# Kernel optimization log

Hardware: AMD Instinct MI355X
Metric: run time of the kernel (lower is better)

Reference implementation:

```python
import jax, jax.numpy as jnp
import numpy as np

H = 512
E = 300
V = 32000
B, L, T = 32, 64, 32

def setup_inputs() -> dict:
    key = jax.random.key(0)
    ks = jax.random.split(key, 24)
    n = jax.random.normal
    inp = {
        "enc_h": n(ks[0], (B, L, 2 * H), jnp.float32),
        "prev_s": n(ks[1], (B, H), jnp.float32),
        "target_word": jax.random.randint(ks[2], (B, T), 0, V),
        # frozen embedding table
        "embed": n(ks[3], (V, E), jnp.float32) * 0.1,
        # attention: W_a (HxH), U_a (2H->H), linear (H->1)
        "W_a": n(ks[4], (H, H), jnp.float32) * 0.001,
        "b_a": jnp.zeros((H,), jnp.float32),
        "U_a": n(ks[5], (2 * H, H), jnp.float32) * 0.001,
        "b_Ua": jnp.zeros((H,), jnp.float32),
        "v_w": n(ks[6], (H,), jnp.float32) * 0.01,
        "v_b": jnp.zeros((1,), jnp.float32),
        # decoder cell, gates stacked as [z | r | s] along output dim
        "W_emb": n(ks[7], (E, 3 * H), jnp.float32) * 0.01,
        "b_emb": jnp.zeros((3 * H,), jnp.float32),
        "W_hid_zr": n(ks[8], (H, 2 * H), jnp.float32) * 0.01,
        "b_hid_zr": jnp.zeros((2 * H,), jnp.float32),
        "W_hid_s": n(ks[9], (H, H), jnp.float32) * 0.01,
        "b_hid_s": jnp.zeros((H,), jnp.float32),
        "W_ctx": n(ks[10], (2 * H, 3 * H), jnp.float32) * 0.01,
        "b_ctx": jnp.zeros((3 * H,), jnp.float32),
        # hid2word
        "W_out": n(ks[11], (H, V), jnp.float32) * 0.02,
        "b_out": jnp.zeros((V,), jnp.float32),
    }
    return inp

def _decode(enc_h, prev_s, target_word, embed, W_a, b_a, U_a, b_Ua, v_w, v_b,
            W_emb, b_emb, W_hid_zr, b_hid_zr, W_hid_s, b_hid_s, W_ctx, b_ctx,
            W_out, b_out):
    # enc_h: B x L x 2H. Precompute U_a(enc_h) once (loop-invariant).
    Uh = jnp.einsum('bld,dh->blh', enc_h, U_a) + b_Ua  # B x L x H
    target_emb = embed[target_word]                    # B x T x E (frozen)

    def step(s, emb_t):
        # Bahdanau attention
        out_s = s @ W_a + b_a                                   # B x H
        scores = jnp.tanh(out_s[:, None, :] + Uh) @ v_w + v_b   # B x L
        attn = jax.nn.softmax(scores, axis=1)                   # B x L
        ctx = jnp.einsum('bld,bl->bd', enc_h, attn)             # B x 2H
        # GRU-like cell, gates stacked [z | r | s]
        ge = emb_t @ W_emb + b_emb          # B x 3H
        gh = s @ W_hid_zr + b_hid_zr        # B x 2H (z, r)
        gc = ctx @ W_ctx + b_ctx            # B x 3H
        z = jax.nn.sigmoid(ge[:, :H] + gh[:, :H] + gc[:, :H])
        r = jax.nn.sigmoid(ge[:, H:2 * H] + gh[:, H:] + gc[:, H:2 * H])
        s_tilde = jnp.tanh(ge[:, 2 * H:] + (r * s) @ W_hid_s + b_hid_s + gc[:, 2 * H:])
        s_new = (1.0 - z) * s + z * s_tilde
        return s_new, s_new

    _, s_seq = jax.lax.scan(step, prev_s, jnp.swapaxes(target_emb, 0, 1))
    s_seq = jnp.swapaxes(s_seq, 0, 1)                # B x T x H
    return jnp.einsum('bth,hv->btv', s_seq, W_out) + b_out  # B x T x V

def reference(enc_h, prev_s, target_word, embed, W_a, b_a, U_a, b_Ua, v_w, v_b,
              W_emb, b_emb, W_hid_zr, b_hid_zr, W_hid_s, b_hid_s, W_ctx, b_ctx,
              W_out, b_out):
    return _decode(enc_h, prev_s, target_word, embed, W_a, b_a, U_a, b_Ua, v_w, v_b,
                   W_emb, b_emb, W_hid_zr, b_hid_zr, W_hid_s, b_hid_s, W_ctx, b_ctx,
                   W_out, b_out)
```

## Files before the change

kernel.cpp:

```cpp
#include <hip/hip_runtime.h>
#include <cstdint>

#define HH   512
#define HD2  1024
#define HD3  1536
#define EE   300
#define VV   32000
#define BB   32
#define LLn  64
#define TT   32

typedef unsigned short u16;
typedef __attribute__((ext_vector_type(8))) short short8;
typedef __attribute__((ext_vector_type(4))) float f32x4;

__device__ __forceinline__ float fast_tanh(float x) {
    float e = __expf(2.f * x);
    return 1.f - 2.f / (e + 1.f);
}
__device__ __forceinline__ float fast_sigmoid(float x) {
    float e = __expf(-x);
    return 1.f / (1.f + e);
}
__device__ __forceinline__ u16 f2bf(float x) {
    union { float f; unsigned u; } v; v.f = x;
    unsigned r = v.u + 0x7FFFu + ((v.u >> 16) & 1u);
    return (u16)(r >> 16);
}

__global__ __launch_bounds__(256) void conv_hilo(
    const float* __restrict__ src, const int* __restrict__ gather,
    int rows_out, int cols_out, int rows_valid, int cols_valid,
    u16* __restrict__ hi, u16* __restrict__ lo)
{
    int idx = blockIdx.x * 256 + threadIdx.x;
    if (idx >= rows_out * cols_out) return;
    int r = idx / cols_out, c = idx - r * cols_out;
    float x = 0.f;
    if (r < rows_valid && c < cols_valid) {
        int sr = gather ? gather[r] : r;
        x = src[(size_t)sr * cols_valid + c];
    }
    union { float f; unsigned u; } v; v.f = x;
    unsigned uh = v.u & 0xFFFF0000u;
    float res = x - __uint_as_float(uh);
    union { float f; unsigned u; } w; w.f = res;
    hi[idx] = (u16)(v.u >> 16);
    lo[idx] = (u16)(w.u >> 16);
}

template<int KSTEPS>
__global__ __launch_bounds__(256) void pre_mfma(
    const u16* __restrict__ Ahi, const u16* __restrict__ Alo,
    const u16* __restrict__ Whi, const u16* __restrict__ Wlo,
    const float* __restrict__ bias, float* __restrict__ C, int N)
{
    __shared__ u16 ah[256 * 40], al[256 * 40];
    __shared__ u16 bh[64 * 40],  bl[64 * 40];
    const int nb = blockIdx.x, mb = blockIdx.y, tid = threadIdx.x;
    const int w = tid >> 6, ln = tid & 63;
    const int quad = ln >> 4, lm = ln & 15;
    const int n0 = nb * 64;
    const int K = KSTEPS * 32;

    f32x4 acc[4][4];
#pragma unroll
    for (int r = 0; r < 4; r++)
#pragma unroll
        for (int c = 0; c < 4; c++)
            acc[r][c] = (f32x4){0.f, 0.f, 0.f, 0.f};

    for (int kt = 0; kt < KSTEPS; kt++) {
        const int k0 = kt * 32;
        {
            const uint4* sh = (const uint4*)(Ahi + (size_t)(mb * 256 + tid) * K + k0);
            const uint4* sl = (const uint4*)(Alo + (size_t)(mb * 256 + tid) * K + k0);
            uint4 h0 = sh[0], h1 = sh[1], h2 = sh[2], h3 = sh[3];
            uint4 l0 = sl[0], l1 = sl[1], l2 = sl[2], l3 = sl[3];
            uint4* dh = (uint4*)(ah + tid * 40);
            dh[0] = h0; dh[1] = h1; dh[2] = h2; dh[3] = h3;
            uint4* dl = (uint4*)(al + tid * 40);
            dl[0] = l0; dl[1] = l1; dl[2] = l2; dl[3] = l3;
        }
        {
            const int kr = tid >> 3, c8 = (tid & 7) * 8;
            union { uint4 v; u16 u[8]; } uh, ul;
            uh.v = *(const uint4*)(Whi + (size_t)(k0 + kr) * N + n0 + c8);
            ul.v = *(const uint4*)(Wlo + (size_t)(k0 + kr) * N + n0 + c8);
#pragma unroll
            for (int j = 0; j < 8; j++) {
                bh[(c8 + j) * 40 + kr] = uh.u[j];
                bl[(c8 + j) * 40 + kr] = ul.u[j];
            }
        }
        __syncthreads();
        short8 afh[4], afl[4], bfh[4], bfl[4];
#pragma unroll
        for (int r = 0; r < 4; r++) {
            afh[r] = *(const short8*)(ah + ((w * 4 + r) * 16 + lm) * 40 + quad * 8);
            afl[r] = *(const short8*)(al + ((w * 4 + r) * 16 + lm) * 40 + quad * 8);
        }
#pragma unroll
        for (int c = 0; c < 4; c++) {
            bfh[c] = *(const short8*)(bh + (c * 16 + lm) * 40 + quad * 8);
            bfl[c] = *(const short8*)(bl + (c * 16 + lm) * 40 + quad * 8);
        }
#pragma unroll
        for (int r = 0; r < 4; r++)
#pragma unroll
            for (int c = 0; c < 4; c++) {
                acc[r][c] = __builtin_amdgcn_mfma_f32_16x16x32_bf16(
                    afh[r], bfh[c], acc[r][c], 0, 0, 0);
                acc[r][c] = __builtin_amdgcn_mfma_f32_16x16x32_bf16(
                    afh[r], bfl[c], acc[r][c], 0, 0, 0);
                acc[r][c] = __builtin_amdgcn_mfma_f32_16x16x32_bf16(
                    afl[r], bfh[c], acc[r][c], 0, 0, 0);
            }
        __syncthreads();
    }
#pragma unroll
    for (int r = 0; r < 4; r++) {
        int row = mb * 256 + (w * 4 + r) * 16 + quad * 4;
#pragma unroll
        for (int c = 0; c < 4; c++) {
            int col = n0 + c * 16 + lm;
            float bo = bias[col];
#pragma unroll
            for (int q2 = 0; q2 < 4; q2++)
                C[(size_t)(row + q2) * N + col] = acc[r][c][q2] + bo;
        }
    }
}

__global__ __launch_bounds__(256) void step_a(
    const float* __restrict__ s_buf, const float* __restrict__ W_a,
    const float* __restrict__ W_hzr, float* __restrict__ parts1)
{
    __shared__ float s_lds[64 * 8];
    const int jt = blockIdx.x, p = blockIdx.y, bq = blockIdx.z;
    const int tid = threadIdx.x;
    const int kk  = tid & 63, blq = tid >> 6;
    const int k0  = p * 64, b0 = bq * 8;

#pragma unroll
    for (int i = 0; i < 2; i++) {
        int bl = blq * 2 + i;
        s_lds[kk * 8 + bl] = s_buf[(b0 + bl) * HH + k0 + kk];
    }
    __syncthreads();

    const int j = jt * 256 + tid;
    const float* Wp; int ld;
    if (j < HH) { Wp = W_a + j;          ld = HH;  }
    else        { Wp = W_hzr + (j - HH); ld = HD2; }
    Wp += (size_t)k0 * ld;

    float acc[8];
#pragma unroll
    for (int r = 0; r < 8; r++) acc[r] = 0.f;
    for (int k = 0; k < 64; k++) {
        float w = Wp[(size_t)k * ld];
#pragma unroll
        for (int r = 0; r < 2; r++) {
            float4 s4 = *(const float4*)(s_lds + k * 8 + r * 4);
            acc[r * 4 + 0] = fmaf(s4.x, w, acc[r * 4 + 0]);
            acc[r * 4 + 1] = fmaf(s4.y, w, acc[r * 4 + 1]);
            acc[r * 4 + 2] = fmaf(s4.z, w, acc[r * 4 + 2]);
            acc[r * 4 + 3] = fmaf(s4.w, w, acc[r * 4 + 3]);
        }
    }
#pragma unroll
    for (int r = 0; r < 8; r++)
        parts1[((size_t)p * BB + b0 + r) * HD3 + j] = acc[r];
}

__global__ __launch_bounds__(256) void step_b(
    const float* __restrict__ parts1, const float* __restrict__ Uh,
    const float* __restrict__ Gc, const float* __restrict__ Ge,
    const float* __restrict__ W_hs,
    const float* __restrict__ b_a, const float* __restrict__ v_w,
    const float* __restrict__ v_b, const float* __restrict__ b_hzr,
    const float* __restrict__ b_hs,
    const float* __restrict__ s_prev, float* __restrict__ s_next,
    u16* __restrict__ sseq, int t)
{
    const int b = blockIdx.x, q = blockIdx.y, tid = threadIdx.x;
    __shared__ float outs[HH];
    __shared__ float red[256];
    __shared__ float attn_s[LLn];
    __shared__ float rs_s[HH];
    __shared__ float zb_s[128], pst_s[128];

    for (int h = tid; h < HH; h += 256) {
        float a = b_a[h];
#pragma unroll
        for (int p = 0; p < 8; p++)
            a += parts1[((size_t)p * BB + b) * HD3 + h];
        outs[h] = a;
    }
    __syncthreads();

    {
        const int l = tid & 63, jj = tid >> 6;
        const float* uh = Uh + ((size_t)b * LLn + l) * HH + jj * 128;
        const float* os = outs + jj * 128;
        const float* vw = v_w + jj * 128;
        float acc = 0.f;
#pragma unroll 8
        for (int i = 0; i < 128; i++)
            acc = fmaf(fast_tanh(os[i] + uh[i]), vw[i], acc);
        red[tid] = acc;
    }
    __syncthreads();

    if (tid < 64) {
        float v = red[tid] + red[64 + tid] + red[128 + tid] + red[192 + tid] + v_b[0];
        float m = v;
        for (int o = 32; o > 0; o >>= 1) m = fmaxf(m, __shfl_xor(m, o));
        float e = __expf(v - m);
        float s = e;
        for (int o = 32; o > 0; o >>= 1) s += __shfl_xor(s, o);
        attn_s[tid] = e / s;
    }
    __syncthreads();

    const float* ge = Ge + (size_t)(b * TT + t) * HD3;

    {
        float g1a = 0.f, g1b = 0.f;
        const float* gc = Gc + (size_t)b * LLn * HD3 + HH;
#pragma unroll 4
        for (int l = 0; l < LLn; l++) {
            float a = attn_s[l];
            g1a = fmaf(a, gc[(size_t)l * HD3 + tid],       g1a);
            g1b = fmaf(a, gc[(size_t)l * HD3 + tid + 256], g1b);
        }
        float gra = b_hzr[HH + tid]       + ge[HH + tid]       + g1a;
        float grb = b_hzr[HH + tid + 256] + ge[HH + tid + 256] + g1b;
#pragma unroll
        for (int p = 0; p < 8; p++) {
            const float* pp = parts1 + ((size_t)p * BB + b) * HD3;
            gra += pp[HD2 + tid];
            grb += pp[HD2 + tid + 256];
        }
        rs_s[tid]       = fast_sigmoid(gra) * s_prev[b * HH + tid];
        rs_s[tid + 256] = fast_sigmoid(grb) * s_prev[b * HH + tid + 256];
    }

    {
        const int hq = q * 128 + (tid & 127);
        if (tid < 128) {
            float g0 = 0.f;
            const float* gc = Gc + (size_t)b * LLn * HD3;
#pragma unroll 4
            for (int l = 0; l < LLn; l++)
                g0 = fmaf(attn_s[l], gc[(size_t)l * HD3 + hq], g0);
            float gz = b_hzr[hq] + ge[hq] + g0;
#pragma unroll
            for (int p = 0; p < 8; p++)
                gz += parts1[((size_t)p * BB + b) * HD3 + HH + hq];
            zb_s[tid] = fast_sigmoid(gz);
        } else {
            float g2 = 0.f;
            const float* gc = Gc + (size_t)b * LLn * HD3 + HD2;
#pragma unroll 4
            for (int l = 0; l < LLn; l++)
                g2 = fmaf(attn_s[l], gc[(size_t)l * HD3 + hq], g2);
            pst_s[tid - 128] = ge[HD2 + hq] + g2 + b_hs[hq];
        }
    }
    __syncthreads();

    {
        const int c = tid & 127, half = tid >> 7;
        const int h0 = q * 128 + c;
        const float* wp = W_hs + (size_t)(half * 256) * HH + h0;
        const float* rp = rs_s + half * 256;
        float a0 = 0.f, a1 = 0.f, a2 = 0.f, a3 = 0.f;
#pragma unroll 4
        for (int k = 0; k < 256; k += 4) {
            a0 = fmaf(rp[k + 0], wp[(size_t)(k + 0) * HH], a0);
            a1 = fmaf(rp[k + 1], wp[(size_t)(k + 1) * HH], a1);
            a2 = fmaf(rp[k + 2], wp[(size_t)(k + 2) * HH], a2);
            a3 = fmaf(rp[k + 3], wp[(size_t)(k + 3) * HH], a3);
        }
        red[tid] = (a0 + a1) + (a2 + a3);
    }
    __syncthreads();

    if (tid < 128) {
        const int h0 = q * 128 + tid;
        float tot = red[tid] + red[128 + tid];
        float st  = fast_tanh(pst_s[tid] + tot);
        float sv  = s_prev[b * HH + h0];
        float sn  = fmaf(zb_s[tid], st - sv, sv);
        s_next[b * HH + h0] = sn;
        sseq[((size_t)b * TT + t) * HH + h0] = f2bf(sn);
    }
}

__global__ __launch_bounds__(256) void final_gemm(
    const u16* __restrict__ Abf, const float* __restrict__ Wout,
    const float* __restrict__ b_out, float* __restrict__ out)
{
    __shared__ u16 a_lds[256 * 40];
    __shared__ u16 b_lds[64 * 40];
    const int nb = blockIdx.x, mb = blockIdx.y, tid = threadIdx.x;
    const int w = tid >> 6, ln = tid & 63;
    const int quad = ln >> 4, lm = ln & 15;
    const int n0 = nb * 64;

    f32x4 acc[4][4];
#pragma unroll
    for (int r = 0; r < 4; r++)
#pragma unroll
        for (int c = 0; c < 4; c++)
            acc[r][c] = (f32x4){0.f, 0.f, 0.f, 0.f};

    for (int kt = 0; kt < 16; kt++) {
        const int k0 = kt * 32;
        {
            const uint4* src = (const uint4*)(Abf + ((size_t)(mb * 256 + tid)) * HH + k0);
            uint4 v0 = src[0], v1 = src[1], v2 = src[2], v3 = src[3];
            uint4* dst = (uint4*)(a_lds + tid * 40);
            dst[0] = v0; dst[1] = v1; dst[2] = v2; dst[3] = v3;
        }
        {
            int kr = tid >> 3, c8 = (tid & 7) * 8;
            const float4* wp = (const float4*)(Wout + (size_t)(k0 + kr) * VV + n0 + c8);
            float4 f0 = wp[0], f1 = wp[1];
            u16 u[8] = { f2bf(f0.x), f2bf(f0.y), f2bf(f0.z), f2bf(f0.w),
                         f2bf(f1.x), f2bf(f1.y), f2bf(f1.z), f2bf(f1.w) };
#pragma unroll
            for (int j = 0; j < 8; j++)
                b_lds[(c8 + j) * 40 + kr] = u[j];
        }
        __syncthreads();
        short8 af[4], bfr[4];
#pragma unroll
        for (int r = 0; r < 4; r++)
            af[r] = *(const short8*)(a_lds + ((w * 4 + r) * 16 + lm) * 40 + quad * 8);
#pragma unroll
        for (int c = 0; c < 4; c++)
            bfr[c] = *(const short8*)(b_lds + (c * 16 + lm) * 40 + quad * 8);
#pragma unroll
        for (int r = 0; r < 4; r++)
#pragma unroll
            for (int c = 0; c < 4; c++)
                acc[r][c] = __builtin_amdgcn_mfma_f32_16x16x32_bf16(
                    af[r], bfr[c], acc[r][c], 0, 0, 0);
        __syncthreads();
    }
#pragma unroll
    for (int r = 0; r < 4; r++) {
        int row = mb * 256 + (w * 4 + r) * 16 + quad * 4;
#pragma unroll
        for (int c = 0; c < 4; c++) {
            int col = n0 + c * 16 + lm;
            float bo = b_out[col];
#pragma unroll
            for (int q = 0; q < 4; q++)
                out[(size_t)(row + q) * VV + col] = acc[r][c][q] + bo;
        }
    }
}

extern "C" void kernel_launch(void* const* d_in, const int* in_sizes, int n_in,
                              void* d_out, int out_size, void* d_ws, size_t ws_size,
                              hipStream_t stream)
{
    const float* enc_h  = (const float*)d_in[0];
    const float* prev_s = (const float*)d_in[1];
    const int*   tw     = (const int*)  d_in[2];
    const float* embed  = (const float*)d_in[3];
    const float* W_a    = (const float*)d_in[4];
    const float* b_a    = (const float*)d_in[5];
    const float* U_a    = (const float*)d_in[6];
    const float* b_Ua   = (const float*)d_in[7];
    const float* v_w    = (const float*)d_in[8];
    const float* v_b    = (const float*)d_in[9];
    const float* W_emb  = (const float*)d_in[10];
    const float* b_emb  = (const float*)d_in[11];
    const float* W_hzr  = (const float*)d_in[12];
    const float* b_hzr  = (const float*)d_in[13];
    const float* W_hs   = (const float*)d_in[14];
    const float* b_hs   = (const float*)d_in[15];
    const float* W_ctx  = (const float*)d_in[16];
    const float* b_ctx  = (const float*)d_in[17];
    const float* W_out  = (const float*)d_in[18];
    const float* b_out  = (const float*)d_in[19];
    float* out = (float*)d_out;

    float* ws = (float*)d_ws;
    float* Uh     = ws;  ws += 2048 * 512;
    float* Gc     = ws;  ws += 2048 * 1536;
    float* Ge     = ws;  ws += 1024 * 1536;
    float* parts1 = ws;  ws += 8 * 32 * 1536;
    float* s0     = ws;  ws += 32 * 512;
    float* s1     = ws;  ws += 32 * 512;
    u16* sseq = (u16*)ws;  ws += (1024 * 512) / 2;
    u16* EHhi = (u16*)ws;  ws += (2048 * 1024) / 2;
    u16* EHlo = (u16*)ws;  ws += (2048 * 1024) / 2;
    u16* UAhi = (u16*)ws;  ws += (1024 * 512) / 2;
    u16* UAlo = (u16*)ws;  ws += (1024 * 512) / 2;
    u16* WChi = (u16*)ws;  ws += (1024 * 1536) / 2;
    u16* WClo = (u16*)ws;  ws += (1024 * 1536) / 2;
    u16* WEhi = (u16*)ws;  ws += (320 * 1536) / 2;
    u16* WElo = (u16*)ws;  ws += (320 * 1536) / 2;
    u16* AGhi = (u16*)ws;  ws += (1024 * 320) / 2;
    u16* AGlo = (u16*)ws;  ws += (1024 * 320) / 2;

    hipMemcpyAsync(s0, prev_s, (size_t)BB * HH * sizeof(float),
                   hipMemcpyDeviceToDevice, stream);

    conv_hilo<<<dim3(8192), 256, 0, stream>>>(enc_h, nullptr, 2048, 1024, 2048, 1024, EHhi, EHlo);
    conv_hilo<<<dim3(2048), 256, 0, stream>>>(U_a,   nullptr, 1024, 512,  1024, 512,  UAhi, UAlo);
    conv_hilo<<<dim3(6144), 256, 0, stream>>>(W_ctx, nullptr, 1024, 1536, 1024, 1536, WChi, WClo);
    conv_hilo<<<dim3(1920), 256, 0, stream>>>(W_emb, nullptr, 320,  1536, 300,  1536, WEhi, WElo);
    conv_hilo<<<dim3(1280), 256, 0, stream>>>(embed, tw,      1024, 320,  1024, 300,  AGhi, AGlo);

    pre_mfma<32><<<dim3(8, 8),  256, 0, stream>>>(EHhi, EHlo, UAhi, UAlo, b_Ua,  Uh, 512);
    pre_mfma<32><<<dim3(24, 8), 256, 0, stream>>>(EHhi, EHlo, WChi, WClo, b_ctx, Gc, 1536);
    pre_mfma<10><<<dim3(24, 4), 256, 0, stream>>>(AGhi, AGlo, WEhi, WElo, b_emb, Ge, 1536);

    for (int t = 0; t < TT; t++) {
        float* sA = (t & 1) ? s1 : s0;
        float* sB = (t & 1) ? s0 : s1;
        step_a<<<dim3(6, 8, 4), 256, 0, stream>>>(sA, W_a, W_hzr, parts1);
        step_b<<<dim3(32, 4), 256, 0, stream>>>(parts1, Uh, Gc, Ge, W_hs,
                                                b_a, v_w, v_b, b_hzr, b_hs,
                                                sA, sB, sseq, t);
    }
    final_gemm<<<dim3(500, 4), 256, 0, stream>>>(sseq, W_out, b_out, out);
}
```

Before: 1.600 ms.

## Use MFMA for recurrent gate GEMM, bf16 intermediates, pre-transposed W_out

```diff
diff --git a/kernel.cpp b/kernel.cpp
--- a/kernel.cpp
+++ b/kernel.cpp
@@ -27,6 +27,20 @@
     unsigned r = v.u + 0x7FFFu + ((v.u >> 16) & 1u);
     return (u16)(r >> 16);
 }
+__device__ __forceinline__ u16 f_hi_trunc(float x) {
+    union { float f; unsigned u; } v; v.f = x;
+    return (u16)(v.u >> 16);
+}
+__device__ __forceinline__ u16 f_lo_trunc(float x) {
+    union { float f; unsigned u; } v; v.f = x;
+    float res = x - __uint_as_float(v.u & 0xFFFF0000u);
+    union { float f; unsigned u; } w; w.f = res;
+    return (u16)(w.u >> 16);
+}
+__device__ __forceinline__ float bf2f(u16 x) {
+    union { unsigned u; float f; } v; v.u = ((unsigned)x) << 16;
+    return v.f;
+}
 
 __global__ __launch_bounds__(256) void conv_hilo(
     const float* __restrict__ src, const int* __restrict__ gather,
@@ -41,19 +55,59 @@
         int sr = gather ? gather[r] : r;
         x = src[(size_t)sr * cols_valid + c];
     }
-    union { float f; unsigned u; } v; v.f = x;
-    unsigned uh = v.u & 0xFFFF0000u;
-    float res = x - __uint_as_float(uh);
-    union { float f; unsigned u; } w; w.f = res;
-    hi[idx] = (u16)(v.u >> 16);
-    lo[idx] = (u16)(w.u >> 16);
-}
-
-template<int KSTEPS>
+    hi[idx] = f_hi_trunc(x);
+    lo[idx] = f_lo_trunc(x);
+}
+
+__global__ __launch_bounds__(256) void conv_bf16(
+    const float* __restrict__ src, u16* __restrict__ dst, int n)
+{
+    int idx = blockIdx.x * 256 + threadIdx.x;
+    if (idx < n) dst[idx] = f2bf(src[idx]);
+}
+
+template<bool HILO>
+__global__ __launch_bounds__(256) void transpose_conv(
+    const float* __restrict__ src, int K, int N, int noff, int dld,
+    u16* __restrict__ dhi, u16* __restrict__ dlo)
+{
+    __shared__ float t[64][65];
+    const int nt = blockIdx.x, ktile = blockIdx.y, tid = threadIdx.x;
+    const int n0 = nt * 64, k0 = ktile * 64;
+#pragma unroll 4
+    for (int i = 0; i < 16; i++) {
+        int kr = i * 4 + (tid >> 6);
+        int nc = tid & 63;
+        t[kr][nc] = src[(size_t)(k0 + kr) * N + n0 + nc];
+    }
+    __syncthreads();
+    const int n = tid >> 2, kc = (tid & 3) * 16;
+    unsigned wh[8], wl[8];
+#pragma unroll
+    for (int jj = 0; jj < 8; jj++) {
+        float x0 = t[kc + 2 * jj][n], x1 = t[kc + 2 * jj + 1][n];
+        if (HILO) {
+            wh[jj] = (unsigned)f_hi_trunc(x0) | ((unsigned)f_hi_trunc(x1) << 16);
+            wl[jj] = (unsigned)f_lo_trunc(x0) | ((unsigned)f_lo_trunc(x1) << 16);
+        } else {
+            wh[jj] = (unsigned)f2bf(x0) | ((unsigned)f2bf(x1) << 16);
+        }
+    }
+    u16* dh = dhi + (size_t)(noff + n0 + n) * dld + k0 + kc;
+    *(uint4*)(dh)     = (uint4){wh[0], wh[1], wh[2], wh[3]};
+    *(uint4*)(dh + 8) = (uint4){wh[4], wh[5], wh[6], wh[7]};
+    if (HILO) {
+        u16* dl = dlo + (size_t)(noff + n0 + n) * dld + k0 + kc;
+        *(uint4*)(dl)     = (uint4){wl[0], wl[1], wl[2], wl[3]};
+        *(uint4*)(dl + 8) = (uint4){wl[4], wl[5], wl[6], wl[7]};
+    }
+}
+
+template<int KSTEPS, bool BF16OUT>
 __global__ __launch_bounds__(256) void pre_mfma(
     const u16* __restrict__ Ahi, const u16* __restrict__ Alo,
     const u16* __restrict__ Whi, const u16* __restrict__ Wlo,
-    const float* __restrict__ bias, float* __restrict__ C, int N)
+    const float* __restrict__ bias, void* __restrict__ Cout, int N)
 {
     __shared__ u16 ah[256 * 40], al[256 * 40];
     __shared__ u16 bh[64 * 40],  bl[64 * 40];
@@ -126,95 +180,103 @@
             int col = n0 + c * 16 + lm;
             float bo = bias[col];
 #pragma unroll
-            for (int q2 = 0; q2 < 4; q2++)
-                C[(size_t)(row + q2) * N + col] = acc[r][c][q2] + bo;
-        }
-    }
-}
-
-__global__ __launch_bounds__(256) void step_a(
-    const float* __restrict__ s_buf, const float* __restrict__ W_a,
-    const float* __restrict__ W_hzr, float* __restrict__ parts1)
-{
-    __shared__ float s_lds[64 * 8];
-    const int jt = blockIdx.x, p = blockIdx.y, bq = blockIdx.z;
-    const int tid = threadIdx.x;
-    const int kk  = tid & 63, blq = tid >> 6;
-    const int k0  = p * 64, b0 = bq * 8;
-
-#pragma unroll
-    for (int i = 0; i < 2; i++) {
-        int bl = blq * 2 + i;
-        s_lds[kk * 8 + bl] = s_buf[(b0 + bl) * HH + k0 + kk];
-    }
-    __syncthreads();
-
-    const int j = jt * 256 + tid;
-    const float* Wp; int ld;
-    if (j < HH) { Wp = W_a + j;          ld = HH;  }
-    else        { Wp = W_hzr + (j - HH); ld = HD2; }
-    Wp += (size_t)k0 * ld;
-
-    float acc[8];
-#pragma unroll
-    for (int r = 0; r < 8; r++) acc[r] = 0.f;
-    for (int k = 0; k < 64; k++) {
-        float w = Wp[(size_t)k * ld];
-#pragma unroll
-        for (int r = 0; r < 2; r++) {
-            float4 s4 = *(const float4*)(s_lds + k * 8 + r * 4);
-            acc[r * 4 + 0] = fmaf(s4.x, w, acc[r * 4 + 0]);
-            acc[r * 4 + 1] = fmaf(s4.y, w, acc[r * 4 + 1]);
-            acc[r * 4 + 2] = fmaf(s4.z, w, acc[r * 4 + 2]);
-            acc[r * 4 + 3] = fmaf(s4.w, w, acc[r * 4 + 3]);
-        }
-    }
-#pragma unroll
-    for (int r = 0; r < 8; r++)
-        parts1[((size_t)p * BB + b0 + r) * HD3 + j] = acc[r];
+            for (int q2 = 0; q2 < 4; q2++) {
+                float val = acc[r][c][q2] + bo;
+                if (BF16OUT)
+                    ((u16*)Cout)[(size_t)(row + q2) * N + col] = f2bf(val);
+                else
+                    ((float*)Cout)[(size_t)(row + q2) * N + col] = val;
+            }
+        }
+    }
+}
+
+__global__ __launch_bounds__(64) void step_a(
+    const u16* __restrict__ shi, const u16* __restrict__ slo, int bstride,
+    const u16* __restrict__ W1hi, const u16* __restrict__ W1lo,
+    float* __restrict__ gates1)
+{
+    const int f = blockIdx.x;
+    const int ln = threadIdx.x;
+    const int quad = ln >> 4, lm = ln & 15;
+    const int n0 = f * 16;
+
+    f32x4 acc0 = (f32x4){0.f, 0.f, 0.f, 0.f};
+    f32x4 acc1 = (f32x4){0.f, 0.f, 0.f, 0.f};
+    const u16* wh  = W1hi + (size_t)(n0 + lm) * 512 + quad * 8;
+    const u16* wl  = W1lo + (size_t)(n0 + lm) * 512 + quad * 8;
+    const u16* ah0 = shi + (size_t)lm * bstride + quad * 8;
+    const u16* al0 = slo + (size_t)lm * bstride + quad * 8;
+    const u16* ah1 = shi + (size_t)(16 + lm) * bstride + quad * 8;
+    const u16* al1 = slo + (size_t)(16 + lm) * bstride + quad * 8;
+
+#pragma unroll
+    for (int kt = 0; kt < 16; kt++) {
+        const int ko = kt * 32;
+        short8 bh  = *(const short8*)(wh + ko);
+        short8 bl  = *(const short8*)(wl + ko);
+        short8 a0h = *(const short8*)(ah0 + ko);
+        short8 a0l = *(const short8*)(al0 + ko);
+        short8 a1h = *(const short8*)(ah1 + ko);
+        short8 a1l = *(const short8*)(al1 + ko);
+        acc0 = __builtin_amdgcn_mfma_f32_16x16x32_bf16(a0h, bh, acc0, 0, 0, 0);
+        acc0 = __builtin_amdgcn_mfma_f32_16x16x32_bf16(a0h, bl, acc0, 0, 0, 0);
+        acc0 = __builtin_amdgcn_mfma_f32_16x16x32_bf16(a0l, bh, acc0, 0, 0, 0);
+        acc1 = __builtin_amdgcn_mfma_f32_16x16x32_bf16(a1h, bh, acc1, 0, 0, 0);
+        acc1 = __builtin_amdgcn_mfma_f32_16x16x32_bf16(a1h, bl, acc1, 0, 0, 0);
+        acc1 = __builtin_amdgcn_mfma_f32_16x16x32_bf16(a1l, bh, acc1, 0, 0, 0);
+    }
+    const int col = n0 + lm;
+#pragma unroll
+    for (int r = 0; r < 4; r++) {
+        gates1[(size_t)(quad * 4 + r) * HD3 + col]        = acc0[r];
+        gates1[(size_t)(16 + quad * 4 + r) * HD3 + col]   = acc1[r];
+    }
 }
 
 __global__ __launch_bounds__(256) void step_b(
-    const float* __restrict__ parts1, const float* __restrict__ Uh,
-    const float* __restrict__ Gc, const float* __restrict__ Ge,
-    const float* __restrict__ W_hs,
+    const float* __restrict__ gates1, const u16* __restrict__ Uh16,
+    const u16* __restrict__ Gc16, const float* __restrict__ Ge,
+    const u16* __restrict__ Whs16,
     const float* __restrict__ b_a, const float* __restrict__ v_w,
     const float* __restrict__ v_b, const float* __restrict__ b_hzr,
     const float* __restrict__ b_hs,
     const float* __restrict__ s_prev, float* __restrict__ s_next,
-    u16* __restrict__ sseq, int t)
-{
-    const int b = blockIdx.x, q = blockIdx.y, tid = threadIdx.x;
-    __shared__ float outs[HH];
+    u16* __restrict__ sseq_hi, u16* __restrict__ sseq_lo, int t)
+{
+    const int q = blockIdx.x, b = blockIdx.y, tid = threadIdx.x;
+    __shared__ float outs_s[HH];
+    __shared__ float vw_s[HH];
     __shared__ float red[256];
     __shared__ float attn_s[LLn];
     __shared__ float rs_s[HH];
     __shared__ float zb_s[128], pst_s[128];
 
-    for (int h = tid; h < HH; h += 256) {
-        float a = b_a[h];
-#pragma unroll
-        for (int p = 0; p < 8; p++)
-            a += parts1[((size_t)p * BB + b) * HD3 + h];
-        outs[h] = a;
-    }
+    outs_s[tid]       = gates1[(size_t)b * HD3 + tid]       + b_a[tid];
+    outs_s[tid + 256] = gates1[(size_t)b * HD3 + tid + 256] + b_a[tid + 256];
+    vw_s[tid]       = v_w[tid];
+    vw_s[tid + 256] = v_w[tid + 256];
     __syncthreads();
 
     {
-        const int l = tid & 63, jj = tid >> 6;
-        const float* uh = Uh + ((size_t)b * LLn + l) * HH + jj * 128;
-        const float* os = outs + jj * 128;
-        const float* vw = v_w + jj * 128;
-        float acc = 0.f;
-#pragma unroll 8
-        for (int i = 0; i < 128; i++)
-            acc = fmaf(fast_tanh(os[i] + uh[i]), vw[i], acc);
-        red[tid] = acc;
+        const int lane = tid & 63, w = tid >> 6;
+        for (int lt = 0; lt < 16; lt++) {
+            const int l = w * 16 + lt;
+            const u16* up = Uh16 + ((size_t)(b * LLn + l)) * HH;
+            float acc = 0.f;
+#pragma unroll
+            for (int j = 0; j < 8; j++) {
+                int hh = j * 64 + lane;
+                acc = fmaf(fast_tanh(outs_s[hh] + bf2f(up[hh])), vw_s[hh], acc);
+            }
+            for (int o = 32; o > 0; o >>= 1) acc += __shfl_xor(acc, o);
+            if (lane == 0) red[l] = acc;
+        }
     }
     __syncthreads();
 
     if (tid < 64) {
-        float v = red[tid] + red[64 + tid] + red[128 + tid] + red[192 + tid] + v_b[0];
+        float v = red[tid] + v_b[0];
         float m = v;
         for (int o = 32; o > 0; o >>= 1) m = fmaxf(m, __shfl_xor(m, o));
         float e = __expf(v - m);
@@ -224,49 +286,43 @@
     }
     __syncthreads();
 
-    const float* ge = Ge + (size_t)(b * TT + t) * HD3;
+    const float* ge = Ge + ((size_t)(b * TT + t)) * HD3;
+    const float* sp = s_prev + b * HH;
 
     {
+        const u16* gc = Gc16 + (size_t)b * LLn * HD3 + HH;
         float g1a = 0.f, g1b = 0.f;
-        const float* gc = Gc + (size_t)b * LLn * HD3 + HH;
 #pragma unroll 4
         for (int l = 0; l < LLn; l++) {
             float a = attn_s[l];
-            g1a = fmaf(a, gc[(size_t)l * HD3 + tid],       g1a);
-            g1b = fmaf(a, gc[(size_t)l * HD3 + tid + 256], g1b);
-        }
-        float gra = b_hzr[HH + tid]       + ge[HH + tid]       + g1a;
-        float grb = b_hzr[HH + tid + 256] + ge[HH + tid + 256] + g1b;
-#pragma unroll
-        for (int p = 0; p < 8; p++) {
-            const float* pp = parts1 + ((size_t)p * BB + b) * HD3;
-            gra += pp[HD2 + tid];
-            grb += pp[HD2 + tid + 256];
-        }
-        rs_s[tid]       = fast_sigmoid(gra) * s_prev[b * HH + tid];
-        rs_s[tid + 256] = fast_sigmoid(grb) * s_prev[b * HH + tid + 256];
-    }
-
+            g1a = fmaf(a, bf2f(gc[(size_t)l * HD3 + tid]),       g1a);
+            g1b = fmaf(a, bf2f(gc[(size_t)l * HD3 + tid + 256]), g1b);
+        }
+        float gra = b_hzr[HH + tid]       + ge[HH + tid]
+                  + gates1[(size_t)b * HD3 + HD2 + tid]       + g1a;
+        float grb = b_hzr[HH + tid + 256] + ge[HH + tid + 256]
+                  + gates1[(size_t)b * HD3 + HD2 + tid + 256] + g1b;
+        rs_s[tid]       = fast_sigmoid(gra) * sp[tid];
+        rs_s[tid + 256] = fast_sigmoid(grb) * sp[tid + 256];
+    }
     {
-        const int hq = q * 128 + (tid & 127);
+        const int c = tid & 127;
+        const int hq = q * 128 + c;
         if (tid < 128) {
+            const u16* gc = Gc16 + (size_t)b * LLn * HD3;
             float g0 = 0.f;
-            const float* gc = Gc + (size_t)b * LLn * HD3;
 #pragma unroll 4
             for (int l = 0; l < LLn; l++)
-                g0 = fmaf(attn_s[l], gc[(size_t)l * HD3 + hq], g0);
-            float gz = b_hzr[hq] + ge[hq] + g0;
-#pragma unroll
-            for (int p = 0; p < 8; p++)
-                gz += parts1[((size_t)p * BB + b) * HD3 + HH + hq];
-            zb_s[tid] = fast_sigmoid(gz);
+                g0 = fmaf(attn_s[l], bf2f(gc[(size_t)l * HD3 + hq]), g0);
+            zb_s[c] = fast_sigmoid(b_hzr[hq] + ge[hq]
+                                   + gates1[(size_t)b * HD3 + HH + hq] + g0);
         } else {
+            const u16* gc = Gc16 + (size_t)b * LLn * HD3 + HD2;
             float g2 = 0.f;
-            const float* gc = Gc + (size_t)b * LLn * HD3 + HD2;
 #pragma unroll 4
             for (int l = 0; l < LLn; l++)
-                g2 = fmaf(attn_s[l], gc[(size_t)l * HD3 + hq], g2);
-            pst_s[tid - 128] = ge[HD2 + hq] + g2 + b_hs[hq];
+                g2 = fmaf(attn_s[l], bf2f(gc[(size_t)l * HD3 + hq]), g2);
+            pst_s[c] = ge[HD2 + hq] + g2 + b_hs[hq];
         }
     }
     __syncthreads();
@@ -274,15 +330,15 @@
     {
         const int c = tid & 127, half = tid >> 7;
         const int h0 = q * 128 + c;
-        const float* wp = W_hs + (size_t)(half * 256) * HH + h0;
+        const u16* wp = Whs16 + (size_t)(half * 256) * HH + h0;
         const float* rp = rs_s + half * 256;
         float a0 = 0.f, a1 = 0.f, a2 = 0.f, a3 = 0.f;
 #pragma unroll 4
         for (int k = 0; k < 256; k += 4) {
-            a0 = fmaf(rp[k + 0], wp[(size_t)(k + 0) * HH], a0);
-            a1 = fmaf(rp[k + 1], wp[(size_t)(k + 1) * HH], a1);
-            a2 = fmaf(rp[k + 2], wp[(size_t)(k + 2) * HH], a2);
-            a3 = fmaf(rp[k + 3], wp[(size_t)(k + 3) * HH], a3);
+            a0 = fmaf(rp[k + 0], bf2f(wp[(size_t)(k + 0) * HH]), a0);
+            a1 = fmaf(rp[k + 1], bf2f(wp[(size_t)(k + 1) * HH]), a1);
+            a2 = fmaf(rp[k + 2], bf2f(wp[(size_t)(k + 2) * HH]), a2);
+            a3 = fmaf(rp[k + 3], bf2f(wp[(size_t)(k + 3) * HH]), a3);
         }
         red[tid] = (a0 + a1) + (a2 + a3);
     }
@@ -290,22 +346,25 @@
 
     if (tid < 128) {
         const int h0 = q * 128 + tid;
-        float tot = red[tid] + red[128 + tid];
-        float st  = fast_tanh(pst_s[tid] + tot);
-        float sv  = s_prev[b * HH + h0];
-        float sn  = fmaf(zb_s[tid], st - sv, sv);
-        s_next[b * HH + h0] = sn;
-        sseq[((size_t)b * TT + t) * HH + h0] = f2bf(sn);
+        float st = fast_tanh(pst_s[tid] + red[tid] + red[128 + tid]);
+        float sv = sp[h0];
+        float sn = fmaf(zb_s[tid], st - sv, sv);
+        s_next[(size_t)b * HH + h0] = sn;
+        size_t off = ((size_t)b * TT + t) * HH + h0;
+        sseq_hi[off] = f_hi_trunc(sn);
+        sseq_lo[off] = f_lo_trunc(sn);
     }
 }
 
 __global__ __launch_bounds__(256) void final_gemm(
-    const u16* __restrict__ Abf, const float* __restrict__ Wout,
-    const float* __restrict__ b_out, float* __restrict__ out)
-{
-    __shared__ u16 a_lds[256 * 40];
+    const u16* __restrict__ Ahi, const u16* __restrict__ Alo,
+    const u16* __restrict__ Wt, const float* __restrict__ b_out,
+    float* __restrict__ out)
+{
+    __shared__ u16 ah_lds[256 * 40];
+    __shared__ u16 al_lds[256 * 40];
     __shared__ u16 b_lds[64 * 40];
-    const int nb = blockIdx.x, mb = blockIdx.y, tid = threadIdx.x;
+    const int mb = blockIdx.x, nb = blockIdx.y, tid = threadIdx.x;
     const int w = tid >> 6, ln = tid & 63;
     const int quad = ln >> 4, lm = ln & 15;
     const int n0 = nb * 64;
@@ -320,35 +379,39 @@
     for (int kt = 0; kt < 16; kt++) {
         const int k0 = kt * 32;
         {
-            const uint4* src = (const uint4*)(Abf + ((size_t)(mb * 256 + tid)) * HH + k0);
-            uint4 v0 = src[0], v1 = src[1], v2 = src[2], v3 = src[3];
-            uint4* dst = (uint4*)(a_lds + tid * 40);
-            dst[0] = v0; dst[1] = v1; dst[2] = v2; dst[3] = v3;
+            const uint4* sh = (const uint4*)(Ahi + (size_t)(mb * 256 + tid) * HH + k0);
+            const uint4* sl = (const uint4*)(Alo + (size_t)(mb * 256 + tid) * HH + k0);
+            uint4 h0 = sh[0], h1 = sh[1], h2 = sh[2], h3 = sh[3];
+            uint4 l0 = sl[0], l1 = sl[1], l2 = sl[2], l3 = sl[3];
+            uint4* dh = (uint4*)(ah_lds + tid * 40);
+            dh[0] = h0; dh[1] = h1; dh[2] = h2; dh[3] = h3;
+            uint4* dl = (uint4*)(al_lds + tid * 40);
+            dl[0] = l0; dl[1] = l1; dl[2] = l2; dl[3] = l3;
         }
         {
-            int kr = tid >> 3, c8 = (tid & 7) * 8;
-            const float4* wp = (const float4*)(Wout + (size_t)(k0 + kr) * VV + n0 + c8);
-            float4 f0 = wp[0], f1 = wp[1];
-            u16 u[8] = { f2bf(f0.x), f2bf(f0.y), f2bf(f0.z), f2bf(f0.w),
-                         f2bf(f1.x), f2bf(f1.y), f2bf(f1.z), f2bf(f1.w) };
-#pragma unroll
-            for (int j = 0; j < 8; j++)
-                b_lds[(c8 + j) * 40 + kr] = u[j];
+            const int n = tid >> 2, part = tid & 3;
+            uint4 v = *(const uint4*)(Wt + (size_t)(n0 + n) * HH + k0 + part * 8);
+            *(uint4*)(b_lds + n * 40 + part * 8) = v;
         }
         __syncthreads();
-        short8 af[4], bfr[4];
-#pragma unroll
-        for (int r = 0; r < 4; r++)
-            af[r] = *(const short8*)(a_lds + ((w * 4 + r) * 16 + lm) * 40 + quad * 8);
+        short8 afh[4], afl[4], bfr[4];
+#pragma unroll
+        for (int r = 0; r < 4; r++) {
+            afh[r] = *(const short8*)(ah_lds + ((w * 4 + r) * 16 + lm) * 40 + quad * 8);
+            afl[r] = *(const short8*)(al_lds + ((w * 4 + r) * 16 + lm) * 40 + quad * 8);
+        }
 #pragma unroll
         for (int c = 0; c < 4; c++)
             bfr[c] = *(const short8*)(b_lds + (c * 16 + lm) * 40 + quad * 8);
 #pragma unroll
         for (int r = 0; r < 4; r++)
 #pragma unroll
-            for (int c = 0; c < 4; c++)
+            for (int c = 0; c < 4; c++) {
                 acc[r][c] = __builtin_amdgcn_mfma_f32_16x16x32_bf16(
-                    af[r], bfr[c], acc[r][c], 0, 0, 0);
+                    afh[r], bfr[c], acc[r][c], 0, 0, 0);
+                acc[r][c] = __builtin_amdgcn_mfma_f32_16x16x32_bf16(
+                    afl[r], bfr[c], acc[r][c], 0, 0, 0);
+            }
         __syncthreads();
     }
 #pragma unroll
@@ -392,13 +455,16 @@
     float* out = (float*)d_out;
 
     float* ws = (float*)d_ws;
-    float* Uh     = ws;  ws += 2048 * 512;
-    float* Gc     = ws;  ws += 2048 * 1536;
     float* Ge     = ws;  ws += 1024 * 1536;
-    float* parts1 = ws;  ws += 8 * 32 * 1536;
+    float* gates1 = ws;  ws += 32 * 1536;
     float* s0     = ws;  ws += 32 * 512;
     float* s1     = ws;  ws += 32 * 512;
-    u16* sseq = (u16*)ws;  ws += (1024 * 512) / 2;
+    u16* Uh16 = (u16*)ws;  ws += (2048 * 512) / 2;
+    u16* Gc16 = (u16*)ws;  ws += (2048 * 1536) / 2;
+    u16* sqh  = (u16*)ws;  ws += (1024 * 512) / 2;
+    u16* sql  = (u16*)ws;  ws += (1024 * 512) / 2;
+    u16* p0hi = (u16*)ws;  ws += (32 * 512) / 2;
+    u16* p0lo = (u16*)ws;  ws += (32 * 512) / 2;
     u16* EHhi = (u16*)ws;  ws += (2048 * 1024) / 2;
     u16* EHlo = (u16*)ws;  ws += (2048 * 1024) / 2;
     u16* UAhi = (u16*)ws;  ws += (1024 * 512) / 2;
@@ -409,27 +475,37 @@
     u16* WElo = (u16*)ws;  ws += (320 * 1536) / 2;
     u16* AGhi = (u16*)ws;  ws += (1024 * 320) / 2;
     u16* AGlo = (u16*)ws;  ws += (1024 * 320) / 2;
-
-    hipMemcpyAsync(s0, prev_s, (size_t)BB * HH * sizeof(float),
-                   hipMemcpyDeviceToDevice, stream);
-
+    u16* W1hi = (u16*)ws;  ws += (1536 * 512) / 2;
+    u16* W1lo = (u16*)ws;  ws += (1536 * 512) / 2;
+    u16* Wt   = (u16*)ws;  ws += (32000 * 512) / 2;
+    u16* Whs16= (u16*)ws;  ws += (512 * 512) / 2;
+
+    conv_hilo<<<dim3(64),   256, 0, stream>>>(prev_s, nullptr, 32, 512, 32, 512, p0hi, p0lo);
     conv_hilo<<<dim3(8192), 256, 0, stream>>>(enc_h, nullptr, 2048, 1024, 2048, 1024, EHhi, EHlo);
     conv_hilo<<<dim3(2048), 256, 0, stream>>>(U_a,   nullptr, 1024, 512,  1024, 512,  UAhi, UAlo);
     conv_hilo<<<dim3(6144), 256, 0, stream>>>(W_ctx, nullptr, 1024, 1536, 1024, 1536, WChi, WClo);
     conv_hilo<<<dim3(1920), 256, 0, stream>>>(W_emb, nullptr, 320,  1536, 300,  1536, WEhi, WElo);
     conv_hilo<<<dim3(1280), 256, 0, stream>>>(embed, tw,      1024, 320,  1024, 300,  AGhi, AGlo);
-
-    pre_mfma<32><<<dim3(8, 8),  256, 0, stream>>>(EHhi, EHlo, UAhi, UAlo, b_Ua,  Uh, 512);
-    pre_mfma<32><<<dim3(24, 8), 256, 0, stream>>>(EHhi, EHlo, WChi, WClo, b_ctx, Gc, 1536);
-    pre_mfma<10><<<dim3(24, 4), 256, 0, stream>>>(AGhi, AGlo, WEhi, WElo, b_emb, Ge, 1536);
+    conv_bf16<<<dim3(1024), 256, 0, stream>>>(W_hs, Whs16, 512 * 512);
+    transpose_conv<true><<<dim3(8, 8),   256, 0, stream>>>(W_a,   512, 512,   0,   512, W1hi, W1lo);
+    transpose_conv<true><<<dim3(16, 8),  256, 0, stream>>>(W_hzr, 512, 1024,  512, 512, W1hi, W1lo);
+    transpose_conv<false><<<dim3(500, 8),256, 0, stream>>>(W_out, 512, 32000, 0,   512, Wt, nullptr);
+
+    pre_mfma<32, true ><<<dim3(8, 8),  256, 0, stream>>>(EHhi, EHlo, UAhi, UAlo, b_Ua,  Uh16, 512);
+    pre_mfma<32, true ><<<dim3(24, 8), 256, 0, stream>>>(EHhi, EHlo, WChi, WClo, b_ctx, Gc16, 1536);
+    pre_mfma<10, false><<<dim3(24, 4), 256, 0, stream>>>(AGhi, AGlo, WEhi, WElo, b_emb, Ge,   1536);
 
     for (int t = 0; t < TT; t++) {
-        float* sA = (t & 1) ? s1 : s0;
-        float* sB = (t & 1) ? s0 : s1;
-        step_a<<<dim3(6, 8, 4), 256, 0, stream>>>(sA, W_a, W_hzr, parts1);
-        step_b<<<dim3(32, 4), 256, 0, stream>>>(parts1, Uh, Gc, Ge, W_hs,
+        const u16* shi; const u16* slo; int bstride;
+        if (t == 0) { shi = p0hi; slo = p0lo; bstride = 512; }
+        else        { shi = sqh + (size_t)(t - 1) * 512;
+                      slo = sql + (size_t)(t - 1) * 512; bstride = TT * 512; }
+        const float* s_in = (t == 0) ? prev_s : ((t & 1) ? s0 : s1);
+        float* s_out = (t & 1) ? s1 : s0;
+        step_a<<<dim3(96), 64, 0, stream>>>(shi, slo, bstride, W1hi, W1lo, gates1);
+        step_b<<<dim3(4, 32), 256, 0, stream>>>(gates1, Uh16, Gc16, Ge, Whs16,
                                                 b_a, v_w, v_b, b_hzr, b_hs,
-                                                sA, sB, sseq, t);
-    }
-    final_gemm<<<dim3(500, 4), 256, 0, stream>>>(sseq, W_out, b_out, out);
-}
+                                                s_in, s_out, sqh, sql, t);
+    }
+    final_gemm<<<dim3(4, 500), 256, 0, stream>>>(sqh, sql, Wt, b_out, out);
+}
```

New measurement: 1.708 ms. 1.07x slower.
